# Kernel tuning notes

Hardware: AMD Instinct MI355X
Metric: run time of the kernel (lower is better)

Reference implementation:

```python
import jax, jax.numpy as jnp
import numpy as np

D_IN = 1024
D_OUT = 1024

def setup_inputs() -> dict:
    key = jax.random.key(0)
    kx, kq, kk, kv = jax.random.split(key, 4)
    X = jax.random.normal(kx, (4, 2048, D_IN), dtype=jnp.float32)
    s = 1.0 / np.sqrt(D_IN)
    Wq = jax.random.uniform(kq, (D_IN, D_OUT), jnp.float32, -s, s)
    Wk = jax.random.uniform(kk, (D_IN, D_OUT), jnp.float32, -s, s)
    Wv = jax.random.uniform(kv, (D_IN, D_OUT), jnp.float32, -s, s)
    return {"X": X, "Wq": Wq, "Wk": Wk, "Wv": Wv}

def reference(X, Wq, Wk, Wv):
    # X: [b, s, d_in]; W*: [d_in, d_out] (torch Linear weight transposed)
    B, S, _ = X.shape
    q = jnp.einsum('bsd,de->bse', X, Wq)
    k = jnp.einsum('bsd,de->bse', X, Wk)
    v = jnp.einsum('bsd,de->bse', X, Wv)
    scores = jnp.einsum('bqe,bke->bqk', q, k)  # [b, s, s]
    causal = jnp.triu(jnp.ones((S, S), dtype=bool), k=1)
    scores = jnp.where(causal, -jnp.inf, scores)
    weights = jax.nn.softmax(scores / jnp.sqrt(jnp.asarray(k.shape[-1], scores.dtype)), axis=-1)
    # dropout p=0.0 (eval) -> identity
    return jnp.einsum('bqk,bke->bqe', weights, v)
```

## Files before the change

### kernel.cpp

```cpp
#include <hip/hip_runtime.h>
#include <cstdint>
#include <cmath>

typedef unsigned short u16;
typedef u16   u16x4  __attribute__((ext_vector_type(4)));
typedef u16   u16x8  __attribute__((ext_vector_type(8)));
typedef __bf16 bf16x8 __attribute__((ext_vector_type(8)));
typedef float f32x4  __attribute__((ext_vector_type(4)));

__device__ __forceinline__ u16 f2bf(float f) {
    uint32_t u = __builtin_bit_cast(uint32_t, f);
    u += 0x7fffu + ((u >> 16) & 1u);
    return (u16)(u >> 16);
}
__device__ __forceinline__ float bf2f(u16 v) {
    uint32_t u = ((uint32_t)v) << 16;
    return __builtin_bit_cast(float, u);
}
__device__ __forceinline__ void gload_lds16(const u16* g, u16* l) {
    __builtin_amdgcn_global_load_lds((const __attribute__((address_space(1))) void*)g,
                                     (__attribute__((address_space(3))) void*)l,
                                     16, 0, 0);
}

__global__ __launch_bounds__(256) void prep_kernel(const float* __restrict__ X,
                                                   const float* __restrict__ Wq,
                                                   const float* __restrict__ Wk,
                                                   const float* __restrict__ Wv,
                                                   u16* __restrict__ Xb,
                                                   u16* __restrict__ Wt) {
    __shared__ u16 tile[64 * 72];
    typedef float f4 __attribute__((ext_vector_type(4)));
    const int bid = blockIdx.x;
    if (bid < 8192) {
        const int idx = bid * 256 + threadIdx.x;
        f4 f = ((const f4*)X)[idx];
        u16x4 o;
        o[0] = f2bf(f[0]); o[1] = f2bf(f[1]); o[2] = f2bf(f[2]); o[3] = f2bf(f[3]);
        ((u16x4*)Xb)[idx] = o;
        return;
    }
    const int id = bid - 8192;
    const int z = id >> 8, rem = id & 255;
    const float* W = (z == 0) ? Wq : (z == 1) ? Wk : Wv;
    u16* out = Wt + ((size_t)z << 20);
    const int nt = (rem & 15) * 64, kt = (rem >> 4) * 64;
    const int t = threadIdx.x, r = t >> 2, cq = (t & 3) * 16;
    const float* src = W + (size_t)(kt + r) * 1024 + nt + cq;
#pragma unroll
    for (int q = 0; q < 4; q++) {
        f4 f = ((const f4*)src)[q];
        tile[r * 72 + cq + q * 4 + 0] = f2bf(f[0]);
        tile[r * 72 + cq + q * 4 + 1] = f2bf(f[1]);
        tile[r * 72 + cq + q * 4 + 2] = f2bf(f[2]);
        tile[r * 72 + cq + q * 4 + 3] = f2bf(f[3]);
    }
    __syncthreads();
    u16x8 o0, o1;
#pragma unroll
    for (int e = 0; e < 8; e++) { o0[e] = tile[(cq + e) * 72 + r]; o1[e] = tile[(cq + 8 + e) * 72 + r]; }
    u16* dst = out + (size_t)(nt + r) * 1024 + kt + cq;
    *(u16x8*)dst = o0;
    *(u16x8*)(dst + 8) = o1;
}

template <int OUTMODE>
__device__ __forceinline__ void gemm_bt_core(u16* __restrict__ smem,
                                             const u16* __restrict__ A,
                                             const u16* __restrict__ Bt,
                                             void* __restrict__ outp,
                                             const int ldk, const int ldo,
                                             const int kbeg, const int kend,
                                             const int m0, const int n0,
                                             const int om0, const int on0) {
    u16* As = smem;
    u16* Bs = smem + 4096;
    const int tid = (int)threadIdx.x;
    const int wave = tid >> 6, lane = tid & 63;
    const int wm = wave >> 1, wn = wave & 1;

    f32x4 acc[4][4] = {};

    const int sr = lane >> 2;
    const int scw = ((lane & 3) ^ ((sr >> 1) & 3)) * 8;
    const u16* gA = A  + (size_t)(m0 + wave * 32 + sr) * ldk + scw;
    const u16* gB = Bt + (size_t)(n0 + wave * 32 + sr) * ldk + scw;
    u16* lA = As + wave * 1024;
    u16* lB = Bs + wave * 1024;
    const size_t rstep = (size_t)ldk * 16;

    const int arow = lane & 15;
    const int ksw  = (arow >> 1) & 3;
    const int koff = (((lane >> 4) ^ ksw)) * 8;
    const u16* pa = As + (wm * 64 + arow) * 32 + koff;
    const u16* pb = Bs + (wn * 64 + arow) * 32 + koff;

    for (int k0 = kbeg; k0 < kend; k0 += 32) {
        gload_lds16(gA + k0,         lA);
        gload_lds16(gA + k0 + rstep, lA + 512);
        gload_lds16(gB + k0,         lB);
        gload_lds16(gB + k0 + rstep, lB + 512);
        __syncthreads();
        bf16x8 a[4], b[4];
#pragma unroll
        for (int i = 0; i < 4; i++) a[i] = *(const bf16x8*)(pa + i * 512);
#pragma unroll
        for (int j = 0; j < 4; j++) b[j] = *(const bf16x8*)(pb + j * 512);
#pragma unroll
        for (int i = 0; i < 4; i++)
#pragma unroll
            for (int j = 0; j < 4; j++)
                acc[i][j] = __builtin_amdgcn_mfma_f32_16x16x32_bf16(a[i], b[j], acc[i][j], 0, 0, 0);
        __syncthreads();
    }

    const int row0 = om0 + wm * 64 + ((lane >> 4) << 2);
    const int col0 = on0 + wn * 64 + (lane & 15);
    if constexpr (OUTMODE == 0) {
        u16* o = (u16*)outp;
#pragma unroll
        for (int i = 0; i < 4; i++)
#pragma unroll
            for (int r = 0; r < 4; r++) {
                u16* po = o + (size_t)(row0 + i * 16 + r) * ldo + col0;
#pragma unroll
                for (int j = 0; j < 4; j++) po[j * 16] = f2bf(acc[i][j][r]);
            }
    } else {
        float* o = (float*)outp;
#pragma unroll
        for (int i = 0; i < 4; i++)
#pragma unroll
            for (int r = 0; r < 4; r++) {
                float* po = o + (size_t)(row0 + i * 16 + r) * ldo + col0;
#pragma unroll
                for (int j = 0; j < 4; j++) po[j * 16] = acc[i][j][r];
            }
    }
}

__global__ __launch_bounds__(256) void qkv_gemm_kernel(const u16* __restrict__ Xb,
                                                       const u16* __restrict__ Wt,
                                                       u16* __restrict__ QKV) {
    __shared__ u16 smem[8192];
    const int bid = blockIdx.x;
    const int xcd = bid & 7, slot = bid >> 3;
    const int z = slot >> 6;
    const int rem = slot & 63;
    const int yl = rem >> 3, x = rem & 7;
    const int y = (xcd << 3) | yl;
    gemm_bt_core<0>(smem, Xb, Wt + ((size_t)z << 20), QKV + ((size_t)z << 23),
                    1024, 1024, 0, 1024, y * 128, x * 128, y * 128, x * 128);
}

__global__ __launch_bounds__(256) void s_tr_kernel(const u16* __restrict__ QKV,
                                                   u16* __restrict__ S,
                                                   u16* __restrict__ Vt) {
    __shared__ u16 smem[8192];
    const int bid = blockIdx.x;
    if (bid < 576) {
        const int xcd = bid & 7, slot = bid >> 3;
        const int b = xcd >> 1, half = xcd & 1;
        int it = half ? 11 : 0;
        const int ntiles = half ? 70 : 66;
        if (slot >= ntiles) return;
        int acc = 0;
        while (acc + it + 1 <= slot) { acc += it + 1; it++; }
        const int jt = slot - acc;
        const u16* Q  = QKV + ((size_t)b << 21);
        const u16* Kp = QKV + ((size_t)1 << 23) + ((size_t)b << 21);
        gemm_bt_core<0>(smem, Q, Kp, S + ((size_t)b << 22), 1024, 2048, 0, 1024,
                        it * 128, jt * 128, it * 128, jt * 128);
        return;
    }
    const int id = bid - 576;
    const int z = id >> 9, rem = id & 511;
    const u16* src = QKV + ((size_t)2 << 23) + ((size_t)z << 21);
    u16* dst = Vt + ((size_t)z << 21);
    const int st = (rem & 31) * 64, et = (rem >> 5) * 64;
    u16 (*tile)[72] = (u16(*)[72])smem;
    const int t = threadIdx.x, r = t >> 2, cq = (t & 3) * 16;
    const u16* p = src + (size_t)(st + r) * 1024 + et + cq;
    u16x8 u0 = *(const u16x8*)p;
    u16x8 u1 = *(const u16x8*)(p + 8);
#pragma unroll
    for (int e = 0; e < 8; e++) { tile[r][cq + e] = u0[e]; tile[r][cq + 8 + e] = u1[e]; }
    __syncthreads();
    u16x8 o0, o1;
#pragma unroll
    for (int e = 0; e < 8; e++) { o0[e] = tile[cq + e][r]; o1[e] = tile[cq + 8 + e][r]; }
    u16* q = dst + (size_t)(et + r) * 2048 + st + cq;
    *(u16x8*)q = o0;
    *(u16x8*)(q + 8) = o1;
}

__global__ __launch_bounds__(256) void pv_gemm_kernel(const u16* __restrict__ P,
                                                      const u16* __restrict__ Vt,
                                                      float* __restrict__ O,
                                                      float* __restrict__ Part) {
    __shared__ u16 smem[8192];
    const unsigned char IT[24]   = {15,14, 7,14,13,13,12,12, 15, 6,11,11,10,10, 9, 5,  0, 1, 2, 8, 3, 9, 8, 4};
    const unsigned char KIND[24] = { 1, 1, 0, 2, 1, 2, 1, 2,  2, 0, 1, 2, 1, 2, 1, 0,  0, 0, 0, 2, 0, 2, 1, 0};
    const int j = blockIdx.x;
    const int slot = j >> 5, combo = j & 31;
    const int it = IT[slot], kind = KIND[slot];
    const int b = combo >> 3, n0 = (combo & 7) * 128;
    const int u = it + 1, h = (u + 1) >> 1;
    const int k_lo = (kind == 2) ? h * 128 : 0;
    const int k_hi = (kind == 1) ? h * 128 : u * 128;
    if (kind == 2) {
        float* dst = Part + ((size_t)((it - 8) * 32 + combo) << 14);
        gemm_bt_core<1>(smem, P + ((size_t)b << 22), Vt + ((size_t)b << 21), dst,
                        2048, 128, k_lo, k_hi, it * 128, n0, 0, 0);
    } else {
        gemm_bt_core<1>(smem, P + ((size_t)b << 22), Vt + ((size_t)b << 21),
                        O + ((size_t)b << 21),
                        2048, 1024, k_lo, k_hi, it * 128, n0, it * 128, n0);
    }
}

__global__ __launch_bounds__(256) void reduce_kernel(float* __restrict__ O,
                                                     const float* __restrict__ Part) {
    const int t = blockIdx.x;
    const int tile = t >> 2, q = t & 3;
    const int it = 8 + (tile >> 5), combo = tile & 31;
    const int b = combo >> 3, n0 = (combo & 7) * 128;
    const f32x4* p = (const f32x4*)(Part + ((size_t)tile << 14)) + q * 1024;
    float* o = O + ((size_t)b << 21) + (size_t)(it * 128 + q * 32) * 1024 + n0;
    const int tid = threadIdx.x;
#pragma unroll
    for (int e = 0; e < 4; e++) {
        const int flat = e * 256 + tid;
        const int row = flat >> 5, col = (flat & 31) * 4;
        f32x4 pv = p[flat];
        f32x4* po = (f32x4*)(o + (size_t)row * 1024 + col);
        f32x4 ov = *po;
        ov[0] += pv[0]; ov[1] += pv[1]; ov[2] += pv[2]; ov[3] += pv[3];
        *po = ov;
    }
}

__global__ __launch_bounds__(256) void softmax_kernel(u16* __restrict__ S) {
    const int wave = threadIdx.x >> 6, lane = threadIdx.x & 63;
    const int g = blockIdx.x * 4 + wave;
    const int b = g >> 11, i = g & 2047;
    u16* row = S + ((size_t)b << 22) + ((size_t)i << 11);
    const int n = i + 1;
    const int kend = ((i >> 7) + 1) << 7;
    const int nt_ = (kend + 511) >> 9;
    const float NEG = -1e30f;
    float v[32];
    float m = NEG;
#pragma unroll
    for (int t = 0; t < 4; t++) {
        if (t < nt_) {
            u16x8 u = *(const u16x8*)(row + t * 512 + lane * 8);
#pragma unroll
            for (int e = 0; e < 8; e++) {
                const int col = t * 512 + lane * 8 + e;
                float f = (col < n) ? bf2f(u[e]) : NEG;
                v[t * 8 + e] = f;
                m = fmaxf(m, f);
            }
        }
    }
#pragma unroll
    for (int off = 32; off > 0; off >>= 1) m = fmaxf(m, __shfl_xor(m, off, 64));
    const float sc = 0.03125f * 1.44269504088896f;
    float s = 0.f;
#pragma unroll
    for (int t = 0; t < 4; t++) {
        if (t < nt_) {
#pragma unroll
            for (int e = 0; e < 8; e++) {
                const float x = v[t * 8 + e];
                const float e2 = (x == NEG) ? 0.f : exp2f((x - m) * sc);
                v[t * 8 + e] = e2;
                s += e2;
            }
        }
    }
#pragma unroll
    for (int off = 32; off > 0; off >>= 1) s += __shfl_xor(s, off, 64);
    const float inv = 1.f / s;
#pragma unroll
    for (int t = 0; t < 4; t++) {
        if (t < nt_) {
            u16x8 o;
#pragma unroll
            for (int e = 0; e < 8; e++) o[e] = f2bf(v[t * 8 + e] * inv);
            *(u16x8*)(row + t * 512 + lane * 8) = o;
        }
    }
}

extern "C" void kernel_launch(void* const* d_in, const int* in_sizes, int n_in,
                              void* d_out, int out_size, void* d_ws, size_t ws_size,
                              hipStream_t stream) {
    const float* X  = (const float*)d_in[0];
    const float* Wq = (const float*)d_in[1];
    const float* Wk = (const float*)d_in[2];
    const float* Wv = (const float*)d_in[3];
    float* out = (float*)d_out;

    u16* ws  = (u16*)d_ws;
    u16* Xb  = ws;
    u16* Wt  = Xb + ((size_t)1 << 23);
    u16* QKV = Wt + 3 * ((size_t)1 << 20);
    u16* S   = QKV + 3 * ((size_t)1 << 23);
    u16* Vt  = Xb;
    float* Part = (float*)QKV;

    prep_kernel<<<8960, 256, 0, stream>>>(X, Wq, Wk, Wv, Xb, Wt);
    qkv_gemm_kernel<<<1536, 256, 0, stream>>>(Xb, Wt, QKV);
    s_tr_kernel<<<2624, 256, 0, stream>>>(QKV, S, Vt);
    softmax_kernel<<<2048, 256, 0, stream>>>(S);
    pv_gemm_kernel<<<768, 256, 0, stream>>>(S, Vt, out, Part);
    reduce_kernel<<<1024, 256, 0, stream>>>(out, Part);
}
```

Before: 236.2 us.

## Rewrite QKV GEMM with 256x256 tiles, 8 waves, and pipelined double-buffered LDS

Replaces the 128x128 QKV projection GEMM (1536 blocks of 256 threads) with a 256x256-tile kernel using 512 threads, a 128KB double-buffered LDS with XOR swizzle, and direct global-to-LDS loads interleaved with MFMA quadrants. It also uses s_setprio and explicit vmcnt waits to overlap loads with compute. The aim is higher arithmetic intensity and better latency hiding for this GEMM. The cost is fewer blocks (384) with large LDS use, which limits occupancy, plus more complex hand scheduling.

```diff
diff --git a/kernel.cpp b/kernel.cpp
--- a/kernel.cpp
+++ b/kernel.cpp
@@ -139,18 +139,123 @@
     }
 }
 
-__global__ __launch_bounds__(256) void qkv_gemm_kernel(const u16* __restrict__ Xb,
-                                                       const u16* __restrict__ Wt,
-                                                       u16* __restrict__ QKV) {
-    __shared__ u16 smem[8192];
+__global__ __launch_bounds__(512, 2) void qkv_gemm_kernel(const u16* __restrict__ Xb,
+                                                          const u16* __restrict__ Wt,
+                                                          u16* __restrict__ QKV) {
+    __shared__ u16 lds[65536];
     const int bid = blockIdx.x;
     const int xcd = bid & 7, slot = bid >> 3;
-    const int z = slot >> 6;
-    const int rem = slot & 63;
-    const int yl = rem >> 3, x = rem & 7;
-    const int y = (xcd << 3) | yl;
-    gemm_bt_core<0>(smem, Xb, Wt + ((size_t)z << 20), QKV + ((size_t)z << 23),
-                    1024, 1024, 0, 1024, y * 128, x * 128, y * 128, x * 128);
+    const int z = slot >> 4, r16 = slot & 15;
+    const int m0 = (xcd * 4 + (r16 >> 2)) << 8;
+    const int n0 = (r16 & 3) << 8;
+
+    const u16* __restrict__ A = Xb;
+    const u16* __restrict__ B = Wt + ((size_t)z << 20);
+    u16* __restrict__ C = QKV + ((size_t)z << 23);
+
+    const int tid = (int)threadIdx.x;
+    const int w = tid >> 6, l = tid & 63;
+    const int wm = w >> 2, wn = w & 3;
+
+    const int srow = w * 16 + (l >> 3);
+    const int scol = ((l & 7) ^ ((l >> 3) & 7)) * 8;
+    const u16* gA = A + (size_t)(m0 + srow) * 1024 + scol;
+    const u16* gB = B + (size_t)(n0 + srow) * 1024 + scol;
+    u16* const sA = lds + w * 1024;
+    u16* const sB = lds + 32768 + w * 1024;
+
+    const int c0 = ((l >> 4) ^ (l & 7)) * 8;
+    const u16* const pa_ = lds + (wm * 64 + (l & 15)) * 64;
+    const u16* const pb_ = lds + 32768 + (wn * 32 + (l & 15)) * 64;
+
+    f32x4 acc[2][2][4][2] = {};
+    bf16x8 a[4][2], b0[2][2], b1[2][2];
+
+#define MFMA_ __builtin_amdgcn_mfma_f32_16x16x32_bf16
+#define STG_A(BUF, H, T) \
+    gload_lds16(gA + (size_t)((H) * 128) * 1024 + (T) * 64,       sA + (BUF) + (H) * 8192); \
+    gload_lds16(gA + (size_t)((H) * 128 + 8) * 1024 + (T) * 64,   sA + (BUF) + (H) * 8192 + 512);
+#define STG_B(BUF, H, T) \
+    gload_lds16(gB + (size_t)((H) * 128) * 1024 + (T) * 64,       sB + (BUF) + (H) * 8192); \
+    gload_lds16(gB + (size_t)((H) * 128 + 8) * 1024 + (T) * 64,   sB + (BUF) + (H) * 8192 + 512);
+#define LD_A(BUF, QA) \
+    _Pragma("unroll") for (int m_ = 0; m_ < 4; m_++) { \
+        a[m_][0] = *(const bf16x8*)(pa_ + (BUF) + (QA) * 8192 + m_ * 1024 + c0); \
+        a[m_][1] = *(const bf16x8*)(pa_ + (BUF) + (QA) * 8192 + m_ * 1024 + (c0 ^ 32)); \
+    }
+#define LD_B(BUF, QB, DST) \
+    _Pragma("unroll") for (int n_ = 0; n_ < 2; n_++) { \
+        DST[n_][0] = *(const bf16x8*)(pb_ + (BUF) + (QB) * 8192 + n_ * 1024 + c0); \
+        DST[n_][1] = *(const bf16x8*)(pb_ + (BUF) + (QB) * 8192 + n_ * 1024 + (c0 ^ 32)); \
+    }
+#define MM(QA, QB, BV) \
+    _Pragma("unroll") for (int m_ = 0; m_ < 4; m_++) { \
+        _Pragma("unroll") for (int n_ = 0; n_ < 2; n_++) { \
+            acc[QA][QB][m_][n_] = MFMA_(a[m_][0], BV[n_][0], acc[QA][QB][m_][n_], 0, 0, 0); \
+            acc[QA][QB][m_][n_] = MFMA_(a[m_][1], BV[n_][1], acc[QA][QB][m_][n_], 0, 0, 0); \
+        } \
+    }
+#define VM6 asm volatile("s_waitcnt vmcnt(6)" ::: "memory");
+#define VM0 asm volatile("s_waitcnt vmcnt(0)" ::: "memory");
+#define VMN
+#define BAR __builtin_amdgcn_s_barrier();
+#define PRIO1 __builtin_amdgcn_s_setprio(1);
+#define PRIO0 __builtin_amdgcn_s_setprio(0);
+#define TILE(BUF, OBUF, T1, S1, T2, S2, VM) \
+    LD_A(BUF, 0) LD_B(BUF, 0, b0) \
+    if (S1) { STG_A(OBUF, 1, T1) } \
+    BAR PRIO1 MM(0, 0, b0) PRIO0 BAR \
+    LD_B(BUF, 1, b1) \
+    if (S2) { STG_A(BUF, 0, T2) } \
+    BAR PRIO1 MM(0, 1, b1) PRIO0 BAR \
+    LD_A(BUF, 1) \
+    if (S2) { STG_B(BUF, 0, T2) } \
+    BAR PRIO1 MM(1, 0, b0) PRIO0 BAR \
+    if (S2) { STG_B(BUF, 1, T2) } \
+    VM \
+    BAR PRIO1 MM(1, 1, b1) PRIO0 BAR
+
+    STG_A(0, 0, 0) STG_B(0, 0, 0) STG_B(0, 1, 0) STG_A(0, 1, 0)
+    STG_A(16384, 0, 1) STG_B(16384, 0, 1) STG_B(16384, 1, 1)
+    asm volatile("s_waitcnt vmcnt(6)" ::: "memory");
+    __builtin_amdgcn_s_barrier();
+
+#pragma unroll 1
+    for (int i = 0; i < 7; ++i) {
+        const int t1 = 2 * i + 1, t2 = 2 * i + 2, t3 = 2 * i + 3;
+        TILE(0,     16384, t1, 1, t2, 1, VM6)
+        TILE(16384, 0,     t2, 1, t3, 1, VM6)
+    }
+    TILE(0,     16384, 15, 1, 0, 0, VM0)
+    TILE(16384, 0,     0,  0, 0, 0, VMN)
+
+    const int row0 = m0 + wm * 64 + ((l >> 4) << 2);
+    const int col0 = n0 + wn * 32 + (l & 15);
+#pragma unroll
+    for (int qa = 0; qa < 2; qa++)
+#pragma unroll
+        for (int qb = 0; qb < 2; qb++)
+#pragma unroll
+            for (int m = 0; m < 4; m++)
+#pragma unroll
+                for (int r = 0; r < 4; r++) {
+                    u16* po = C + (size_t)(row0 + qa * 128 + m * 16 + r) * 1024 + col0 + qb * 128;
+#pragma unroll
+                    for (int n = 0; n < 2; n++) po[n * 16] = f2bf(acc[qa][qb][m][n][r]);
+                }
+#undef MFMA_
+#undef STG_A
+#undef STG_B
+#undef LD_A
+#undef LD_B
+#undef MM
+#undef VM6
+#undef VM0
+#undef VMN
+#undef BAR
+#undef PRIO1
+#undef PRIO0
+#undef TILE
 }
 
 __global__ __launch_bounds__(256) void s_tr_kernel(const u16* __restrict__ QKV,
@@ -312,7 +417,7 @@
     float* Part = (float*)QKV;
 
     prep_kernel<<<8960, 256, 0, stream>>>(X, Wq, Wk, Wv, Xb, Wt);
-    qkv_gemm_kernel<<<1536, 256, 0, stream>>>(Xb, Wt, QKV);
+    qkv_gemm_kernel<<<384, 512, 0, stream>>>(Xb, Wt, QKV);
     s_tr_kernel<<<2624, 256, 0, stream>>>(QKV, S, Vt);
     softmax_kernel<<<2048, 256, 0, stream>>>(S);
     pv_gemm_kernel<<<768, 256, 0, stream>>>(S, Vt, out, Part);
```

Measured after the change: 237.6 us. About the same (+0.6%).
